# Kernel optimization log

Measured on AMD Instinct MI355X. Metric: run time of the kernel, lower is better.

## Reference

```python
import jax, jax.numpy as jnp
import numpy as np


def setup_inputs() -> dict:
    key = jax.random.key(0)
    k1, k2, k3, k4 = jax.random.split(key, 4)
    B, H, W = 32, 32, 32
    NUM_CODE, IN_DIM, CODE_DIM = 4096, 1024, 256
    encode = jax.random.normal(k1, (B, H, W, CODE_DIM), dtype=jnp.float32)
    codebook = jax.random.normal(k2, (NUM_CODE, IN_DIM), dtype=jnp.float32)  # nn.init.normal_(std=1)
    proj_w = jax.random.normal(k3, (CODE_DIM, IN_DIM), dtype=jnp.float32) * (1.0 / np.sqrt(IN_DIM))
    proj_b = jax.random.normal(k4, (CODE_DIM,), dtype=jnp.float32) * 0.01
    return {"encode": encode, "codebook": codebook, "proj_w": proj_w, "proj_b": proj_b}


def reference(encode, codebook, proj_w, proj_b):
    # e = project(codebook.weight): (num_code, code_dim)
    e = codebook @ proj_w.T + proj_b
    b, h, w, c = encode.shape
    z = encode.reshape(-1, c)  # (N, code_dim)
    # -cdist(z, e, p=2) via ||z||^2 + ||e||^2 - 2 z.e (computed under no_grad in the original)
    d2 = (
        jnp.sum(z * z, axis=-1, keepdims=True)
        + jnp.sum(e * e, axis=-1)[None, :]
        - 2.0 * (z @ e.T)
    )
    dist = jnp.sqrt(jnp.maximum(d2, 0.0))  # (N, num_code)
    # simi = (-dist - mu)/sigma is a monotone decreasing map of dist, and zidx = argmax(softmax(simi))
    # == argmax(simi) == argmin(dist); softmax/normalization does not affect the returned outputs.
    zidx = jnp.argmin(dist, axis=-1).reshape(b, h, w)  # (b, h, w) int
    quant = e[zidx]  # (b, h, w, code_dim) embedding gather
    return zidx, quant
```

## Files before the change

### kernel.cpp

```cpp
#include <hip/hip_runtime.h>
#include <hip/hip_bf16.h>
#include <stdint.h>

#define NROWS 32768
#define NCODE 4096
#define CDIM  256
#define KDIM  1024
#define NSLOT 96
#define MARGIN 1.0f

typedef __attribute__((ext_vector_type(8))) short bf16x8;
typedef __attribute__((ext_vector_type(4))) float f32x4;

static __device__ __forceinline__ unsigned f2ord(float f) {
    unsigned b = __float_as_uint(f);
    return (b & 0x80000000u) ? ~b : (b | 0x80000000u);
}
static __device__ __forceinline__ float ord2f(unsigned u) {
    unsigned b = (u & 0x80000000u) ? (u ^ 0x80000000u) : ~u;
    return __uint_as_float(b);
}
static __device__ __forceinline__ unsigned short to_bf16(float f) {
    __hip_bfloat16 h = __float2bfloat16(f);
    return *(unsigned short*)&h;
}

extern "C" __global__ __launch_bounds__(256)
void k_proj(const float* __restrict__ cb, const float* __restrict__ pw,
            const float* __restrict__ pb, float* __restrict__ e,
            unsigned short* __restrict__ eb)
{
    __shared__ __align__(16) float As[32][68];
    __shared__ __align__(16) float Bs[32][68];
    const int tid = threadIdx.x;
    const int tx = tid & 15, ty = tid >> 4;
    const int bm = blockIdx.x;
    const int bn = blockIdx.y;
    float acc[4][4] = {};

    float4 pva[2], pvb[2];
    auto issueP = [&](int k0) {
#pragma unroll
        for (int i = 0; i < 2; ++i) {
            int idx = tid + i * 256;
            int row = idx >> 3;
            int kg  = (idx & 7) << 2;
            pva[i] = *(const float4*)(cb + (size_t)(bm * 64 + row) * KDIM + k0 + kg);
            pvb[i] = *(const float4*)(pw + (size_t)(bn * 64 + row) * KDIM + k0 + kg);
        }
    };

    issueP(0);
    for (int k0 = 0; k0 < KDIM; k0 += 32) {
#pragma unroll
        for (int i = 0; i < 2; ++i) {
            int idx = tid + i * 256;
            int row = idx >> 3;
            int kg  = (idx & 7) << 2;
            As[kg + 0][row] = pva[i].x; As[kg + 1][row] = pva[i].y;
            As[kg + 2][row] = pva[i].z; As[kg + 3][row] = pva[i].w;
            Bs[kg + 0][row] = pvb[i].x; Bs[kg + 1][row] = pvb[i].y;
            Bs[kg + 2][row] = pvb[i].z; Bs[kg + 3][row] = pvb[i].w;
        }
        __syncthreads();
        if (k0 + 32 < KDIM) issueP(k0 + 32);
#pragma unroll
        for (int k = 0; k < 32; ++k) {
            float4 a = *(const float4*)&As[k][ty * 4];
            float4 b = *(const float4*)&Bs[k][tx * 4];
            float av[4] = {a.x, a.y, a.z, a.w};
            float bv[4] = {b.x, b.y, b.z, b.w};
#pragma unroll
            for (int i = 0; i < 4; ++i)
#pragma unroll
                for (int j = 0; j < 4; ++j)
                    acc[i][j] = fmaf(av[i], bv[j], acc[i][j]);
        }
        __syncthreads();
    }
    const int col0 = bn * 64 + tx * 4;
    float4 bias = *(const float4*)(pb + col0);
    float bb[4] = {bias.x, bias.y, bias.z, bias.w};
#pragma unroll
    for (int i = 0; i < 4; ++i) {
        int row = bm * 64 + ty * 4 + i;
        float o[4];
#pragma unroll
        for (int j = 0; j < 4; ++j) o[j] = acc[i][j] + bb[j];
        *(float4*)(e + (size_t)row * CDIM + col0) = make_float4(o[0], o[1], o[2], o[3]);
        ushort4 ob;
        ob.x = to_bf16(o[0]); ob.y = to_bf16(o[1]);
        ob.z = to_bf16(o[2]); ob.w = to_bf16(o[3]);
        *(ushort4*)(eb + (size_t)row * CDIM + col0) = ob;
    }
}

extern "C" __global__ __launch_bounds__(256)
void k_enorm(const float* __restrict__ e, float* __restrict__ en)
{
    int code = blockIdx.x * 4 + (threadIdx.x >> 6);
    int lane = threadIdx.x & 63;
    float4 v = *(const float4*)(e + (size_t)code * CDIM + lane * 4);
    float s = v.x * v.x + v.y * v.y + v.z * v.z + v.w * v.w;
#pragma unroll
    for (int off = 1; off < 64; off <<= 1) s += __shfl_xor(s, off);
    if (lane == 0) en[code] = s;
}

extern "C" __global__ __launch_bounds__(256)
void k_cvtz(const float* __restrict__ z, unsigned short* __restrict__ zb,
            unsigned* __restrict__ cnt)
{
    size_t i = (size_t)blockIdx.x * 256 + threadIdx.x;
    if (i < NROWS) cnt[i] = 0u;
    const float4* src = (const float4*)(z + i * 16);
    unsigned short o[16];
#pragma unroll
    for (int q = 0; q < 4; ++q) {
        float4 v = src[q];
        o[q * 4 + 0] = to_bf16(v.x); o[q * 4 + 1] = to_bf16(v.y);
        o[q * 4 + 2] = to_bf16(v.z); o[q * 4 + 3] = to_bf16(v.w);
    }
    *(uint4*)(zb + i * 16)     = *(const uint4*)&o[0];
    *(uint4*)(zb + i * 16 + 8) = *(const uint4*)&o[8];
}

extern "C" __global__ __launch_bounds__(256, 4)
void k_dist(const unsigned short* __restrict__ zb, const unsigned short* __restrict__ eb,
            const float* __restrict__ en, unsigned* __restrict__ cnt,
            unsigned* __restrict__ cand)
{
    __shared__ __align__(16) char lds[32768];
    __shared__ unsigned rowmin[128];
    const int tid  = threadIdx.x;
    const int wave = tid >> 6, lane = tid & 63;
    const int bC = blockIdx.x, bR = blockIdx.y;
    const int wr = wave >> 1, wc = wave & 1;
    const int fr = lane & 15;
    const int kg = (lane >> 4) << 3;
    const int qs = bC & 3;
    if (tid < 128) rowmin[tid] = 0xFFFFFFFFu;

    char* As = lds;
    char* Bs = lds + 16384;
    const char* gz = (const char*)zb + (size_t)bR * 128 * 512;
    const char* ge = (const char*)eb + (size_t)bC * 128 * 512;

    const int colg0 = bC * 128 + wc * 64;
    float env[4];
#pragma unroll
    for (int ni = 0; ni < 4; ++ni) env[ni] = en[colg0 + ni * 16 + fr];

    f32x4 acc[4][4] = {};

    for (int qi = 0; qi < 4; ++qi) {
        const int q = (qs + qi) & 3;
#pragma unroll
        for (int i = 0; i < 4; ++i) {
            int chunk = tid + i * 256;
            int r  = chunk >> 3;
            int wb = (chunk & 7) << 4;
            int sw = wb ^ ((r & 7) << 4);
            const char* gA = gz + (size_t)r * 512 + q * 128 + sw;
            const char* gB = ge + (size_t)r * 512 + q * 128 + sw;
            char* lA = As + i * 4096 + wave * 1024;
            char* lB = Bs + i * 4096 + wave * 1024;
            __builtin_amdgcn_global_load_lds(
                (const __attribute__((address_space(1))) unsigned int*)gA,
                (__attribute__((address_space(3))) unsigned int*)lA, 16, 0, 0);
            __builtin_amdgcn_global_load_lds(
                (const __attribute__((address_space(1))) unsigned int*)gB,
                (__attribute__((address_space(3))) unsigned int*)lB, 16, 0, 0);
        }
        __syncthreads();
#pragma unroll
        for (int ks = 0; ks < 2; ++ks) {
            const int kb = (ks * 32 + kg) * 2;
            bf16x8 a[4], b[4];
#pragma unroll
            for (int mi = 0; mi < 4; ++mi) {
                int row = wr * 64 + mi * 16 + fr;
                a[mi] = *(const bf16x8*)(As + row * 128 + (kb ^ ((row & 7) << 4)));
            }
#pragma unroll
            for (int ni = 0; ni < 4; ++ni) {
                int row = wc * 64 + ni * 16 + fr;
                b[ni] = *(const bf16x8*)(Bs + row * 128 + (kb ^ ((row & 7) << 4)));
            }
#pragma unroll
            for (int mi = 0; mi < 4; ++mi)
#pragma unroll
                for (int ni = 0; ni < 4; ++ni)
                    acc[mi][ni] = __builtin_amdgcn_mfma_f32_16x16x32_bf16(
                        a[mi], b[ni], acc[mi][ni], 0, 0, 0);
        }
        __syncthreads();
    }

#pragma unroll
    for (int mi = 0; mi < 4; ++mi)
#pragma unroll
        for (int ni = 0; ni < 4; ++ni)
#pragma unroll
            for (int j = 0; j < 4; ++j)
                acc[mi][ni][j] = fmaf(-2.0f, acc[mi][ni][j], env[ni]);

#pragma unroll
    for (int mi = 0; mi < 4; ++mi) {
#pragma unroll
        for (int j = 0; j < 4; ++j) {
            unsigned best = 0xFFFFFFFFu;
#pragma unroll
            for (int ni = 0; ni < 4; ++ni) {
                unsigned o = f2ord(acc[mi][ni][j]);
                best = o < best ? o : best;
            }
#pragma unroll
            for (int off = 8; off >= 1; off >>= 1) {
                unsigned o = __shfl_xor(best, off);
                best = o < best ? o : best;
            }
            if (fr == 0) {
                int rl = wr * 64 + mi * 16 + ((lane >> 4) << 2) + j;
                atomicMin(&rowmin[rl], best);
            }
        }
    }
    __syncthreads();

#pragma unroll
    for (int mi = 0; mi < 4; ++mi) {
#pragma unroll
        for (int j = 0; j < 4; ++j) {
            int rl = wr * 64 + mi * 16 + ((lane >> 4) << 2) + j;
            float thr = ord2f(rowmin[rl]) + MARGIN;
#pragma unroll
            for (int ni = 0; ni < 4; ++ni) {
                if (!(acc[mi][ni][j] > thr)) {
                    int rg = bR * 128 + rl;
                    unsigned slot = atomicAdd(&cnt[rg], 1u);
                    if (slot < NSLOT)
                        cand[(size_t)rg * NSLOT + slot] =
                            (unsigned)(colg0 + ni * 16 + fr);
                }
            }
        }
    }
}

extern "C" __global__ __launch_bounds__(256)
void k_rerank(const float* __restrict__ z, const float* __restrict__ e,
              const float* __restrict__ en, const unsigned* __restrict__ cnt,
              const unsigned* __restrict__ cand, unsigned* __restrict__ outidx)
{
    int row  = blockIdx.x * 4 + (threadIdx.x >> 6);
    int lane = threadIdx.x & 63;
    int g    = lane >> 4;
    int sl   = lane & 15;
    const float* zp = z + (size_t)row * CDIM + sl * 16;
    float4 zv[4];
#pragma unroll
    for (int t = 0; t < 4; ++t) zv[t] = *(const float4*)(zp + t * 4);
    unsigned n = cnt[row];
    double best_d2 = 1e300;
    unsigned best_col = 0u;

    auto eval4 = [&](unsigned col, bool valid) {
        const float* ep = e + (size_t)col * CDIM + sl * 16;
        double dot = 0.0;
#pragma unroll
        for (int t = 0; t < 4; ++t) {
            float4 ev = *(const float4*)(ep + t * 4);
            dot += (double)zv[t].x * ev.x + (double)zv[t].y * ev.y
                 + (double)zv[t].z * ev.z + (double)zv[t].w * ev.w;
        }
#pragma unroll
        for (int off = 1; off < 16; off <<= 1) dot += __shfl_xor(dot, off);
        double d2 = valid ? ((double)en[col] - 2.0 * dot) : 1e300;
#pragma unroll
        for (int off = 16; off <= 32; off <<= 1) {
            double od2    = __shfl_xor(d2, off);
            unsigned ocol = (unsigned)__shfl_xor((int)col, off);
            if (od2 < d2 || (od2 == d2 && ocol < col)) { d2 = od2; col = ocol; }
        }
        if (d2 < best_d2 || (d2 == best_d2 && col < best_col)) {
            best_d2 = d2; best_col = col;
        }
    };

    if (n >= 1u && n <= (unsigned)NSLOT) {
        for (unsigned i = 0; i < n; i += 4) {
            unsigned ii = i + (unsigned)g;
            bool valid = ii < n;
            unsigned col = valid ? (cand[(size_t)row * NSLOT + ii] & (NCODE - 1)) : 0u;
            eval4(col, valid);
        }
    } else {
        for (unsigned c0 = 0; c0 < NCODE; c0 += 4)
            eval4(c0 + (unsigned)g, true);
    }
    if (lane == 0) outidx[row] = best_col;
}

extern "C" __global__ __launch_bounds__(256)
void k_out(const unsigned* __restrict__ outidx, const float* __restrict__ e,
           float* __restrict__ out)
{
    int row  = blockIdx.x * 4 + (threadIdx.x >> 6);
    int lane = threadIdx.x & 63;
    unsigned idx = outidx[row] & (NCODE - 1);
    if (lane == 0) out[row] = (float)idx;
    float4 v = *(const float4*)(e + (size_t)idx * CDIM + lane * 4);
    *(float4*)(out + NROWS + (size_t)row * CDIM + lane * 4) = v;
}

extern "C" void kernel_launch(void* const* d_in, const int* in_sizes, int n_in,
                              void* d_out, int out_size, void* d_ws, size_t ws_size,
                              hipStream_t stream)
{
    const float* encode = (const float*)d_in[0];
    const float* cb     = (const float*)d_in[1];
    const float* pw     = (const float*)d_in[2];
    const float* pb     = (const float*)d_in[3];
    float* out = (float*)d_out;

    char* ws = (char*)d_ws;
    float*    e      = (float*)(ws);
    float*    en     = (float*)(ws + (4u << 20));
    unsigned* cnt    = (unsigned*)(ws + (4u << 20) + (16u << 10));
    unsigned* outidx = (unsigned*)(ws + (4u << 20) + (144u << 10));

    char* S = (char*)(out + NROWS);
    unsigned short* zb   = (unsigned short*)(S);
    unsigned short* eb   = (unsigned short*)(S + (16u << 20));
    unsigned*       cand = (unsigned*)(S + (18u << 20));

    k_proj  <<<dim3(64, 4),   256, 0, stream>>>(cb, pw, pb, e, eb);
    k_enorm <<<dim3(1024),    256, 0, stream>>>(e, en);
    k_cvtz  <<<dim3(2048),    256, 0, stream>>>(encode, zb, cnt);
    k_dist  <<<dim3(32, 256), 256, 0, stream>>>(zb, eb, en, cnt, cand);
    k_rerank<<<dim3(8192),    256, 0, stream>>>(encode, e, en, cnt, cand, outidx);
    k_out   <<<dim3(8192),    256, 0, stream>>>(outidx, e, out);
}
```

Before: 364.3 us.

## Fuse projection, codebook norms and z conversion into one prep kernel

Merges the codebook projection GEMM, the codebook squared-norm computation and the z-to-bf16 conversion into a single launch. The projection blocks now write partial norms per column-quarter (en4), which the distance and rerank kernels sum on read. Conversion work runs in extra blocks of the same grid so it overlaps the projection. This removes two kernel launches and the separate pass over e, at the cost of four loads per norm lookup in later kernels.

```diff
diff --git a/kernel.cpp b/kernel.cpp
--- a/kernel.cpp
+++ b/kernel.cpp
@@ -26,16 +26,36 @@
 }
 
 extern "C" __global__ __launch_bounds__(256)
-void k_proj(const float* __restrict__ cb, const float* __restrict__ pw,
-            const float* __restrict__ pb, float* __restrict__ e,
-            unsigned short* __restrict__ eb)
+void k_prep(const float* __restrict__ cb, const float* __restrict__ pw,
+            const float* __restrict__ pb, const float* __restrict__ z,
+            float* __restrict__ e, unsigned short* __restrict__ eb,
+            float* __restrict__ en4, unsigned short* __restrict__ zb,
+            unsigned* __restrict__ cnt)
 {
     __shared__ __align__(16) float As[32][68];
     __shared__ __align__(16) float Bs[32][68];
+    const int blk = blockIdx.x;
     const int tid = threadIdx.x;
+
+    if (blk >= 256) {
+        size_t i = (size_t)(blk - 256) * 256 + tid;
+        if (i < NROWS) cnt[i] = 0u;
+        const float4* src = (const float4*)(z + i * 16);
+        unsigned short o[16];
+#pragma unroll
+        for (int q = 0; q < 4; ++q) {
+            float4 v = src[q];
+            o[q * 4 + 0] = to_bf16(v.x); o[q * 4 + 1] = to_bf16(v.y);
+            o[q * 4 + 2] = to_bf16(v.z); o[q * 4 + 3] = to_bf16(v.w);
+        }
+        *(uint4*)(zb + i * 16)     = *(const uint4*)&o[0];
+        *(uint4*)(zb + i * 16 + 8) = *(const uint4*)&o[8];
+        return;
+    }
+
     const int tx = tid & 15, ty = tid >> 4;
-    const int bm = blockIdx.x;
-    const int bn = blockIdx.y;
+    const int bm = blk >> 2;
+    const int bn = blk & 3;
     float acc[4][4] = {};
 
     float4 pva[2], pvb[2];
@@ -92,42 +112,16 @@
         ob.x = to_bf16(o[0]); ob.y = to_bf16(o[1]);
         ob.z = to_bf16(o[2]); ob.w = to_bf16(o[3]);
         *(ushort4*)(eb + (size_t)row * CDIM + col0) = ob;
-    }
-}
-
-extern "C" __global__ __launch_bounds__(256)
-void k_enorm(const float* __restrict__ e, float* __restrict__ en)
-{
-    int code = blockIdx.x * 4 + (threadIdx.x >> 6);
-    int lane = threadIdx.x & 63;
-    float4 v = *(const float4*)(e + (size_t)code * CDIM + lane * 4);
-    float s = v.x * v.x + v.y * v.y + v.z * v.z + v.w * v.w;
-#pragma unroll
-    for (int off = 1; off < 64; off <<= 1) s += __shfl_xor(s, off);
-    if (lane == 0) en[code] = s;
-}
-
-extern "C" __global__ __launch_bounds__(256)
-void k_cvtz(const float* __restrict__ z, unsigned short* __restrict__ zb,
-            unsigned* __restrict__ cnt)
-{
-    size_t i = (size_t)blockIdx.x * 256 + threadIdx.x;
-    if (i < NROWS) cnt[i] = 0u;
-    const float4* src = (const float4*)(z + i * 16);
-    unsigned short o[16];
-#pragma unroll
-    for (int q = 0; q < 4; ++q) {
-        float4 v = src[q];
-        o[q * 4 + 0] = to_bf16(v.x); o[q * 4 + 1] = to_bf16(v.y);
-        o[q * 4 + 2] = to_bf16(v.z); o[q * 4 + 3] = to_bf16(v.w);
-    }
-    *(uint4*)(zb + i * 16)     = *(const uint4*)&o[0];
-    *(uint4*)(zb + i * 16 + 8) = *(const uint4*)&o[8];
+        float ns = o[0] * o[0] + o[1] * o[1] + o[2] * o[2] + o[3] * o[3];
+#pragma unroll
+        for (int off = 1; off < 16; off <<= 1) ns += __shfl_xor(ns, off);
+        if (tx == 0) en4[bn * NCODE + row] = ns;
+    }
 }
 
 extern "C" __global__ __launch_bounds__(256, 4)
 void k_dist(const unsigned short* __restrict__ zb, const unsigned short* __restrict__ eb,
-            const float* __restrict__ en, unsigned* __restrict__ cnt,
+            const float* __restrict__ en4, unsigned* __restrict__ cnt,
             unsigned* __restrict__ cand)
 {
     __shared__ __align__(16) char lds[32768];
@@ -149,7 +143,10 @@
     const int colg0 = bC * 128 + wc * 64;
     float env[4];
 #pragma unroll
-    for (int ni = 0; ni < 4; ++ni) env[ni] = en[colg0 + ni * 16 + fr];
+    for (int ni = 0; ni < 4; ++ni) {
+        int c = colg0 + ni * 16 + fr;
+        env[ni] = en4[c] + en4[NCODE + c] + en4[2 * NCODE + c] + en4[3 * NCODE + c];
+    }
 
     f32x4 acc[4][4] = {};
 
@@ -250,7 +247,7 @@
 
 extern "C" __global__ __launch_bounds__(256)
 void k_rerank(const float* __restrict__ z, const float* __restrict__ e,
-              const float* __restrict__ en, const unsigned* __restrict__ cnt,
+              const float* __restrict__ en4, const unsigned* __restrict__ cnt,
               const unsigned* __restrict__ cand, unsigned* __restrict__ outidx)
 {
     int row  = blockIdx.x * 4 + (threadIdx.x >> 6);
@@ -276,7 +273,9 @@
         }
 #pragma unroll
         for (int off = 1; off < 16; off <<= 1) dot += __shfl_xor(dot, off);
-        double d2 = valid ? ((double)en[col] - 2.0 * dot) : 1e300;
+        float enc = en4[col] + en4[NCODE + col]
+                  + en4[2 * NCODE + col] + en4[3 * NCODE + col];
+        double d2 = valid ? ((double)enc - 2.0 * dot) : 1e300;
 #pragma unroll
         for (int off = 16; off <= 32; off <<= 1) {
             double od2    = __shfl_xor(d2, off);
@@ -326,19 +325,18 @@
 
     char* ws = (char*)d_ws;
     float*    e      = (float*)(ws);
-    float*    en     = (float*)(ws + (4u << 20));
-    unsigned* cnt    = (unsigned*)(ws + (4u << 20) + (16u << 10));
-    unsigned* outidx = (unsigned*)(ws + (4u << 20) + (144u << 10));
+    float*    en4    = (float*)(ws + (4u << 20));
+    unsigned* cnt    = (unsigned*)(ws + (4u << 20) + (64u << 10));
+    unsigned* outidx = (unsigned*)(ws + (4u << 20) + (192u << 10));
 
     char* S = (char*)(out + NROWS);
     unsigned short* zb   = (unsigned short*)(S);
     unsigned short* eb   = (unsigned short*)(S + (16u << 20));
     unsigned*       cand = (unsigned*)(S + (18u << 20));
 
-    k_proj  <<<dim3(64, 4),   256, 0, stream>>>(cb, pw, pb, e, eb);
-    k_enorm <<<dim3(1024),    256, 0, stream>>>(e, en);
-    k_cvtz  <<<dim3(2048),    256, 0, stream>>>(encode, zb, cnt);
-    k_dist  <<<dim3(32, 256), 256, 0, stream>>>(zb, eb, en, cnt, cand);
-    k_rerank<<<dim3(8192),    256, 0, stream>>>(encode, e, en, cnt, cand, outidx);
+    k_prep  <<<dim3(2304),    256, 0, stream>>>(cb, pw, pb, encode,
+                                                e, eb, en4, zb, cnt);
+    k_dist  <<<dim3(32, 256), 256, 0, stream>>>(zb, eb, en4, cnt, cand);
+    k_rerank<<<dim3(8192),    256, 0, stream>>>(encode, e, en4, cnt, cand, outidx);
     k_out   <<<dim3(8192),    256, 0, stream>>>(outidx, e, out);
 }
```

New measurement: 365.5 us, median of 2. Within noise of the previous version (+0.4%).
